# Kernel tuning notes

Measured on AMD Instinct MI355X. Metric: run time of the kernel, lower is better.

Reference implementation:

```python
import jax, jax.numpy as jnp
import numpy as np

N = 50000
NEG_SLOPE = 0.2  # PyG GATConv default negative_slope


def _gat_layer(x, src, dst, edge_attr, W, We, a_src, a_dst, a_edge, bias):
    """Single-head PyG GATConv (heads=1, concat=True, add_self_loops=True,
    fill_value='mean' for self-loop edge_attr, dropout inactive / eval mode)."""
    n = x.shape[0]
    # add self loops; self-loop edge_attr = per-feature mean of edge_attr
    loop = jnp.arange(n)
    src2 = jnp.concatenate([src, loop])
    dst2 = jnp.concatenate([dst, loop])
    ea_loop = jnp.broadcast_to(edge_attr.mean(axis=0, keepdims=True), (n, edge_attr.shape[1]))
    ea = jnp.concatenate([edge_attr, ea_loop], axis=0)          # [E', edge_dim]

    h = x @ W                                                    # [N, C_out]
    a_s = h @ a_src                                              # [N]
    a_d = h @ a_dst                                              # [N]
    a_e = (ea @ We) @ a_edge                                     # [E']

    alpha = jax.nn.leaky_relu(a_s[src2] + a_d[dst2] + a_e, NEG_SLOPE)  # [E']
    # segment softmax over incoming edges of each dst node
    amax = jax.ops.segment_max(alpha, dst2, num_segments=n)     # [N]
    ex = jnp.exp(alpha - amax[dst2])                             # [E']
    denom = jax.ops.segment_sum(ex, dst2, num_segments=n)       # [N]
    w = ex / denom[dst2]                                         # [E']

    msg = h[src2] * w[:, None]                                   # [E', C_out]
    out = jax.ops.segment_sum(msg, dst2, num_segments=n) + bias  # [N, C_out]
    return out


def setup_inputs() -> dict:
    key = jax.random.key(0)
    ks = jax.random.split(key, 16)
    E, C_in, C_h, C_out, Ed = 800000, 128, 256, 128, 8
    s = 0.05
    inp = {
        "x": jax.random.normal(ks[0], (N, C_in), dtype=jnp.float32),
        "edge_index": jax.random.randint(ks[1], (2, E), 0, N, dtype=jnp.int32),
        "edge_attr": jax.random.normal(ks[2], (E, Ed), dtype=jnp.float32),
        # layer 1 params
        "W1": jax.random.normal(ks[3], (C_in, C_h), dtype=jnp.float32) * s,
        "We1": jax.random.normal(ks[4], (Ed, C_h), dtype=jnp.float32) * s,
        "as1": jax.random.normal(ks[5], (C_h,), dtype=jnp.float32) * s,
        "ad1": jax.random.normal(ks[6], (C_h,), dtype=jnp.float32) * s,
        "ae1": jax.random.normal(ks[7], (C_h,), dtype=jnp.float32) * s,
        "b1": jnp.zeros((C_h,), dtype=jnp.float32),
        # layer 2 params
        "W2": jax.random.normal(ks[8], (C_h, C_out), dtype=jnp.float32) * s,
        "We2": jax.random.normal(ks[9], (Ed, C_out), dtype=jnp.float32) * s,
        "as2": jax.random.normal(ks[10], (C_out,), dtype=jnp.float32) * s,
        "ad2": jax.random.normal(ks[11], (C_out,), dtype=jnp.float32) * s,
        "ae2": jax.random.normal(ks[12], (C_out,), dtype=jnp.float32) * s,
        "b2": jnp.zeros((C_out,), dtype=jnp.float32),
    }
    return inp


def reference(x, edge_index, edge_attr, W1, We1, as1, ad1, ae1, b1,
              W2, We2, as2, ad2, ae2, b2):
    src, dst = edge_index[0], edge_index[1]
    h = _gat_layer(x, src, dst, edge_attr, W1, We1, as1, ad1, ae1, b1)
    h = jax.nn.relu(h)  # relu between layers, not after last
    out = _gat_layer(h, src, dst, edge_attr, W2, We2, as2, ad2, ae2, b2)
    return out
```

## Files before the change

kernel.cpp:

```cpp
#include <hip/hip_runtime.h>
#include <hip/hip_bf16.h>


#define NEG_SLOPE 0.2f

typedef unsigned short u16;
typedef short short8 __attribute__((ext_vector_type(8)));
typedef float v4f __attribute__((ext_vector_type(4)));
typedef u16 u16x8 __attribute__((ext_vector_type(8)));

__device__ __forceinline__ u16 f2bf(float f) {
    unsigned u = __float_as_uint(f);
    return (u16)((u + 0x7fffu + ((u >> 16) & 1u)) >> 16);
}
__device__ __forceinline__ float bf2f(u16 h) {
    return __uint_as_float(((unsigned)h) << 16);
}
__device__ __forceinline__ float bf_lo(int v) { return __uint_as_float(((unsigned)v) << 16); }
__device__ __forceinline__ float bf_hi(int v) { return __uint_as_float(((unsigned)v) & 0xffff0000u); }
__device__ __forceinline__ float lrelu(float x) {
    return x >= 0.f ? x : NEG_SLOPE * x;
}
__device__ __forceinline__ int ld_acq(int* p) {
    return __hip_atomic_load(p, __ATOMIC_ACQUIRE, __HIP_MEMORY_SCOPE_AGENT);
}
__device__ __forceinline__ void st_rel(int* p, int v) {
    __hip_atomic_store(p, v, __ATOMIC_RELEASE, __HIP_MEMORY_SCOPE_AGENT);
}

__global__ __launch_bounds__(256) void prep_kernel(
        const float* __restrict__ W1, u16* __restrict__ w1thi, u16* __restrict__ w1tlo,
        const float* __restrict__ W2, u16* __restrict__ w2thi, u16* __restrict__ w2tlo,
        const float* __restrict__ We1, const float* __restrict__ ae1v,
        const float* __restrict__ We2, const float* __restrict__ ae2v,
        float* __restrict__ we_vec1g, float* __restrict__ we_vec2g) {
    int tid = threadIdx.x;
    if (blockIdx.x < 256) {
        int t = blockIdx.x * 256 + tid;
        if (t < 128 * 256) {
            int k = t >> 8, m = t & 255;
            float v = W1[t];
            u16 h = f2bf(v);
            w1thi[(size_t)m * 128 + k] = h;
            w1tlo[(size_t)m * 128 + k] = f2bf(v - bf2f(h));
        } else {
            t -= 128 * 256;
            int k = t >> 7, m = t & 127;
            float v = W2[t];
            u16 h = f2bf(v);
            w2thi[(size_t)m * 256 + k] = h;
            w2tlo[(size_t)m * 256 + k] = f2bf(v - bf2f(h));
        }
        return;
    }
    __shared__ float wv[16];
    if (tid < 16) wv[tid] = 0.f;
    __syncthreads();
    {
        float a1 = ae1v[tid];
        int lane = tid & 63;
#pragma unroll
        for (int j = 0; j < 8; ++j) {
            float v = We1[j * 256 + tid] * a1;
#pragma unroll
            for (int o = 32; o; o >>= 1) v += __shfl_down(v, o);
            if (lane == 0) atomicAdd(&wv[j], v);
        }
        if (tid < 128) {
            float a2 = ae2v[tid];
#pragma unroll
            for (int j = 0; j < 8; ++j) {
                float v = We2[j * 128 + tid] * a2;
#pragma unroll
                for (int o = 32; o; o >>= 1) v += __shfl_down(v, o);
                if (lane == 0) atomicAdd(&wv[8 + j], v);
            }
        }
    }
    __syncthreads();
    if (tid < 8)  we_vec1g[tid] = wv[tid];
    else if (tid < 16) we_vec2g[tid - 8] = wv[tid];
}

#define BK 32
#define LDA 40
__global__ __launch_bounds__(256) void fat1_kernel(
        const float* __restrict__ ea, const int* __restrict__ dst,
        float* __restrict__ mean_acc, int* __restrict__ deg,
        int* __restrict__ rank, float2* __restrict__ aEe, int E,
        const float* __restrict__ we_vec1g, const float* __restrict__ we_vec2g,
        int Fb, int Gg,
        const float* __restrict__ A32,
        const u16* __restrict__ Bh_g, const u16* __restrict__ Bl_g,
        u16* __restrict__ Cb, int Nrows, int K, int M,
        const float* __restrict__ av, const float* __restrict__ bv,
        float* __restrict__ as_out, float* __restrict__ ad_out, int gx) {
    __shared__ u16 Ah[64 * LDA];
    __shared__ u16 Bh[128 * LDA];
    __shared__ u16 Bl[128 * LDA];
    __shared__ float red[8];
    int tid = threadIdx.x;
    int bid = (int)blockIdx.x;
    int mn = Fb < Gg ? Fb : Gg;
    int hid = -1, gid = -1;
    if (bid < 2 * mn) {
        if ((bid & 1) == 0) hid = bid >> 1; else gid = bid >> 1;
    } else {
        int rem = bid - 2 * mn;
        if (Fb > Gg) hid = mn + rem; else gid = mn + rem;
    }
    if (hid >= 0) {
        float wv[16];
#pragma unroll
        for (int j = 0; j < 8; ++j) { wv[j] = we_vec1g[j]; wv[8 + j] = we_vec2g[j]; }
        if (tid < 8) red[tid] = 0.f;
        __syncthreads();
        float s[8] = {0.f};
        int stride = Fb * 256;
        for (int e = hid * 256 + tid; e < E; e += stride) {
            int d = dst[e];
            const float4 v0 = *(const float4*)&ea[(size_t)e * 8];
            const float4 v1 = *(const float4*)&ea[(size_t)e * 8 + 4];
            s[0] += v0.x; s[1] += v0.y; s[2] += v0.z; s[3] += v0.w;
            s[4] += v1.x; s[5] += v1.y; s[6] += v1.z; s[7] += v1.w;
            float s1 = v0.x * wv[0] + v0.y * wv[1] + v0.z * wv[2] + v0.w * wv[3]
                     + v1.x * wv[4] + v1.y * wv[5] + v1.z * wv[6] + v1.w * wv[7];
            float s2 = v0.x * wv[8] + v0.y * wv[9] + v0.z * wv[10] + v0.w * wv[11]
                     + v1.x * wv[12] + v1.y * wv[13] + v1.z * wv[14] + v1.w * wv[15];
            aEe[e] = make_float2(s1, s2);
            rank[e] = atomicAdd(&deg[d], 1);
        }
        int lane = tid & 63;
#pragma unroll
        for (int j = 0; j < 8; ++j) {
#pragma unroll
            for (int o = 32; o; o >>= 1) s[j] += __shfl_down(s[j], o);
            if (lane == 0) atomicAdd(&red[j], s[j]);
        }
        __syncthreads();
        if (tid < 8) atomicAdd(&mean_acc[tid], red[tid]);
        return;
    }
    int lane = tid & 63;
    int wvx = tid >> 6;
    int l15 = lane & 15, quad = lane >> 4;
    int rb = (gid / gx) * 64;
    int cb = (gid % gx) * 128;

    v4f acc[8];
#pragma unroll
    for (int ni = 0; ni < 8; ++ni) acc[ni] = (v4f){0.f, 0.f, 0.f, 0.f};

    int sr  = tid >> 2;
    int sc  = (tid & 3) * 8;
    int sr2 = tid >> 1;
    int sc2 = (tid & 1) * 16;

    for (int kc = 0; kc < K; kc += BK) {
        int gr = rb + sr;
        u16x8 a0 = {0,0,0,0,0,0,0,0};
        if (gr < Nrows) {
            const float* pa = A32 + (size_t)gr * K + kc + sc;
            float4 f0 = *(const float4*)pa;
            float4 f1 = *(const float4*)(pa + 4);
            a0 = (u16x8){f2bf(f0.x), f2bf(f0.y), f2bf(f0.z), f2bf(f0.w),
                         f2bf(f1.x), f2bf(f1.y), f2bf(f1.z), f2bf(f1.w)};
        }
        size_t bb = (size_t)(cb + sr2) * K + kc + sc2;
        u16x8 b0 = *(const u16x8*)(Bh_g + bb);
        u16x8 b1 = *(const u16x8*)(Bh_g + bb + 8);
        u16x8 b2 = *(const u16x8*)(Bl_g + bb);
        u16x8 b3 = *(const u16x8*)(Bl_g + bb + 8);
        *(u16x8*)&Ah[sr * LDA + sc] = a0;
        *(u16x8*)&Bh[sr2 * LDA + sc2] = b0;
        *(u16x8*)&Bh[sr2 * LDA + sc2 + 8] = b1;
        *(u16x8*)&Bl[sr2 * LDA + sc2] = b2;
        *(u16x8*)&Bl[sr2 * LDA + sc2 + 8] = b3;
        __syncthreads();
        short8 ah = *(const short8*)&Ah[(wvx * 16 + l15) * LDA + quad * 8];
#pragma unroll
        for (int ni = 0; ni < 8; ++ni) {
            int r = (ni * 16 + l15) * LDA + quad * 8;
            short8 bhf = *(const short8*)&Bh[r];
            short8 blf = *(const short8*)&Bl[r];
            acc[ni] = __builtin_amdgcn_mfma_f32_16x16x32_bf16(ah, bhf, acc[ni], 0, 0, 0);
            acc[ni] = __builtin_amdgcn_mfma_f32_16x16x32_bf16(ah, blf, acc[ni], 0, 0, 0);
        }
        __syncthreads();
    }
#pragma unroll
    for (int ni = 0; ni < 8; ++ni)
#pragma unroll
        for (int reg = 0; reg < 4; ++reg) {
            int row = rb + wvx * 16 + quad * 4 + reg;
            if (row < Nrows)
                Cb[(size_t)row * M + cb + ni * 16 + l15] = f2bf(acc[ni][reg]);
        }
    float sd[4] = {}, dd[4] = {};
#pragma unroll
    for (int ni = 0; ni < 8; ++ni) {
        int col = cb + ni * 16 + l15;
        float a = av[col], b = bv[col];
#pragma unroll
        for (int reg = 0; reg < 4; ++reg) {
            sd[reg] += acc[ni][reg] * a;
            dd[reg] += acc[ni][reg] * b;
        }
    }
#pragma unroll
    for (int off = 1; off < 16; off <<= 1)
#pragma unroll
        for (int reg = 0; reg < 4; ++reg) {
            sd[reg] += __shfl_xor(sd[reg], off);
            dd[reg] += __shfl_xor(dd[reg], off);
        }
    if (l15 == 0) {
        int row0 = rb + wvx * 16 + quad * 4;
#pragma unroll
        for (int reg = 0; reg < 4; ++reg)
            if (row0 + reg < Nrows) {
                atomicAdd(as_out + row0 + reg, sd[reg]);
                atomicAdd(ad_out + row0 + reg, dd[reg]);
            }
    }
}

__global__ __launch_bounds__(256) void scan_fused_kernel(
        const int* __restrict__ deg, int* __restrict__ row_start,
        int* __restrict__ partials, int* __restrict__ pprefix,
        int* __restrict__ gcount, int* __restrict__ gflag, int N, int n,
        const float* __restrict__ mean_acc, float Einv,
        const float* __restrict__ we_vec1, const float* __restrict__ we_vec2,
        float* __restrict__ ae_loop) {
    __shared__ int s[256];
    __shared__ int amLast, bprefix;
    int t = threadIdx.x, bid = blockIdx.x;
    int i = bid * 256 + t;
    int v = (i < N) ? deg[i] : 0;
    s[t] = v; __syncthreads();
    for (int off = 1; off < 256; off <<= 1) {
        int u = (t >= off) ? s[t - off] : 0;
        __syncthreads();
        s[t] += u;
        __syncthreads();
    }
    int incl = s[t];
    int total = s[255];
    if (t == 0) {
        partials[bid] = total;
        __threadfence();
        int c = __hip_atomic_fetch_add(gcount, 1, __ATOMIC_ACQ_REL, __HIP_MEMORY_SCOPE_AGENT);
        amLast = (c == (int)gridDim.x - 1);
    }
    __syncthreads();
    if (amLast) {
        int G = gridDim.x;
        int pv = (t < G) ? ld_acq(&partials[t]) : 0;
        __syncthreads();
        s[t] = pv; __syncthreads();
        for (int off = 1; off < 256; off <<= 1) {
            int u = (t >= off) ? s[t - off] : 0;
            __syncthreads();
            s[t] += u;
            __syncthreads();
        }
        if (t < G) pprefix[t] = s[t] - pv;
        if (t == 0) {
            float s1 = 0.f, s2 = 0.f;
#pragma unroll
            for (int j = 0; j < 8; ++j) {
                float m = mean_acc[j] * Einv;
                s1 += m * we_vec1[j];
                s2 += m * we_vec2[j];
            }
            ae_loop[0] = s1; ae_loop[1] = s2;
        }
        __threadfence();
        __syncthreads();
        if (t == 0) st_rel(gflag, 1);
    }
    if (t == 0) {
        while (ld_acq(gflag) == 0) __builtin_amdgcn_s_sleep(2);
        bprefix = ld_acq(&pprefix[bid]);
    }
    __syncthreads();
    int ex = bprefix + incl - v;
    if (i < n) row_start[i] = ex;
}

__global__ __launch_bounds__(256) void fill_kernel(
        const int* __restrict__ src, const int* __restrict__ dst,
        const float2* __restrict__ aEe, const int* __restrict__ row_start,
        const int* __restrict__ rank,
        const float* __restrict__ asv1, const float* __restrict__ adv1,
        float4* __restrict__ epack, int E) {
    int e = blockIdx.x * 256 + threadIdx.x;
    if (e >= E) return;
    int d = dst[e];
    int s = src[e];
    int idx = row_start[d] + rank[e];
    float2 a = aEe[e];
    float w = __expf(lrelu(asv1[s] + adv1[d] + a.x));
    epack[idx] = make_float4(__int_as_float(s), w, a.y, 0.f);
}

#define LDA2 40
__global__ __launch_bounds__(256) void gemm_mfma_kernel(
        const u16* __restrict__ A_g,
        const u16* __restrict__ Bh_g, const u16* __restrict__ Bl_g,
        u16* __restrict__ Cb, int Nrows, int K, int M,
        const float* __restrict__ av, const float* __restrict__ bv,
        float* __restrict__ as_out, float* __restrict__ ad_out) {
    __shared__ u16 Ah[128 * LDA2], Bh[128 * LDA2], Bl[128 * LDA2];
    int tid = threadIdx.x;
    int lane = tid & 63;
    int wv = tid >> 6;
    int wm = wv >> 1, wn = wv & 1;
    int l15 = lane & 15, quad = lane >> 4;
    int rb = blockIdx.y * 128;
    int cb = blockIdx.x * 128;

    v4f acc[4][4];
#pragma unroll
    for (int mi = 0; mi < 4; ++mi)
#pragma unroll
        for (int ni = 0; ni < 4; ++ni) acc[mi][ni] = (v4f){0.f, 0.f, 0.f, 0.f};

    int sr = tid >> 1;
    int sc = (tid & 1) * 16;

    for (int kc = 0; kc < K; kc += BK) {
        int gr = rb + sr;
        u16x8 a0 = {0,0,0,0,0,0,0,0}, a1 = {0,0,0,0,0,0,0,0};
        if (gr < Nrows) {
            size_t ba = (size_t)gr * K + kc + sc;
            a0 = *(const u16x8*)(A_g + ba);
            a1 = *(const u16x8*)(A_g + ba + 8);
        }
        size_t bb = (size_t)(cb + sr) * K + kc + sc;
        u16x8 b0 = *(const u16x8*)(Bh_g + bb);
        u16x8 b1 = *(const u16x8*)(Bh_g + bb + 8);
        u16x8 b2 = *(const u16x8*)(Bl_g + bb);
        u16x8 b3 = *(const u16x8*)(Bl_g + bb + 8);
        *(u16x8*)&Ah[sr * LDA2 + sc] = a0;
        *(u16x8*)&Ah[sr * LDA2 + sc + 8] = a1;
        *(u16x8*)&Bh[sr * LDA2 + sc] = b0;
        *(u16x8*)&Bh[sr * LDA2 + sc + 8] = b1;
        *(u16x8*)&Bl[sr * LDA2 + sc] = b2;
        *(u16x8*)&Bl[sr * LDA2 + sc + 8] = b3;
        __syncthreads();
        short8 ah[4], bh[4], bl[4];
#pragma unroll
        for (int mi = 0; mi < 4; ++mi)
            ah[mi] = *(const short8*)&Ah[(wm * 64 + mi * 16 + l15) * LDA2 + quad * 8];
#pragma unroll
        for (int ni = 0; ni < 4; ++ni) {
            int r = (wn * 64 + ni * 16 + l15) * LDA2 + quad * 8;
            bh[ni] = *(const short8*)&Bh[r];
            bl[ni] = *(const short8*)&Bl[r];
        }
#pragma unroll
        for (int mi = 0; mi < 4; ++mi)
#pragma unroll
            for (int ni = 0; ni < 4; ++ni) {
                acc[mi][ni] = __builtin_amdgcn_mfma_f32_16x16x32_bf16(ah[mi], bh[ni], acc[mi][ni], 0, 0, 0);
                acc[mi][ni] = __builtin_amdgcn_mfma_f32_16x16x32_bf16(ah[mi], bl[ni], acc[mi][ni], 0, 0, 0);
            }
        __syncthreads();
    }
#pragma unroll
    for (int mi = 0; mi < 4; ++mi)
#pragma unroll
        for (int ni = 0; ni < 4; ++ni)
#pragma unroll
            for (int reg = 0; reg < 4; ++reg) {
                int row = rb + wm * 64 + mi * 16 + quad * 4 + reg;
                if (row < Nrows)
                    Cb[(size_t)row * M + cb + wn * 64 + ni * 16 + l15] = f2bf(acc[mi][ni][reg]);
            }
    float sd[4][4] = {}, dd[4][4] = {};
#pragma unroll
    for (int ni = 0; ni < 4; ++ni) {
        int col = cb + wn * 64 + ni * 16 + l15;
        float a = av[col], b = bv[col];
#pragma unroll
        for (int mi = 0; mi < 4; ++mi)
#pragma unroll
            for (int reg = 0; reg < 4; ++reg) {
                sd[mi][reg] += acc[mi][ni][reg] * a;
                dd[mi][reg] += acc[mi][ni][reg] * b;
            }
    }
#pragma unroll
    for (int off = 1; off < 16; off <<= 1)
#pragma unroll
        for (int mi = 0; mi < 4; ++mi)
#pragma unroll
            for (int reg = 0; reg < 4; ++reg) {
                sd[mi][reg] += __shfl_xor(sd[mi][reg], off);
                dd[mi][reg] += __shfl_xor(dd[mi][reg], off);
            }
    if (l15 == 0)
#pragma unroll
        for (int mi = 0; mi < 4; ++mi) {
            int row0 = rb + wm * 64 + mi * 16 + quad * 4;
#pragma unroll
            for (int reg = 0; reg < 4; ++reg)
                if (row0 + reg < Nrows) {
                    atomicAdd(as_out + row0 + reg, sd[mi][reg]);
                    atomicAdd(ad_out + row0 + reg, dd[mi][reg]);
                }
        }
}

__global__ __launch_bounds__(256) void agg1_kernel(const int* __restrict__ row_start,
                                                   const float4* __restrict__ epack,
                                                   const float* __restrict__ asv,
                                                   const float* __restrict__ adv,
                                                   const float* __restrict__ ae_loop,
                                                   const u16* __restrict__ Hb,
                                                   u16* __restrict__ ohi,
                                                   const float* __restrict__ bias, int N) {
    __shared__ float2 xch[4][64];
    int lane = threadIdx.x & 63;
    int wvi = threadIdx.x >> 6;
    int node = blockIdx.x * 4 + wvi;
    if (node >= N) return;
    int st = row_start[node], en = row_start[node + 1];
    float wloop = __expf(lrelu(asv[node] + adv[node] + ae_loop[0]));
    float sum = wloop;
    int half = lane >> 5;
    int hl   = lane & 31;
    float acc[8];
    {
        int4 hv = *(const int4*)(Hb + (size_t)node * 256 + hl * 8);
        float w0 = half ? 0.f : wloop;
        acc[0] = w0 * bf_lo(hv.x); acc[1] = w0 * bf_hi(hv.x);
        acc[2] = w0 * bf_lo(hv.y); acc[3] = w0 * bf_hi(hv.y);
        acc[4] = w0 * bf_lo(hv.z); acc[5] = w0 * bf_hi(hv.z);
        acc[6] = w0 * bf_lo(hv.w); acc[7] = w0 * bf_hi(hv.w);
    }
    for (int base = st; base < en; base += 64) {
        int i = base + lane;
        float w = 0.f; int sreg = 0;
        if (i < en) {
            float4 ep = epack[i];
            sreg = __float_as_int(ep.x);
            w = ep.y;
        }
        float wsum = w;
#pragma unroll
        for (int o = 1; o < 64; o <<= 1) wsum += __shfl_xor(wsum, o);
        sum += wsum;
        xch[wvi][lane] = make_float2(w, __int_as_float(sreg));
        int cnt = min(64, en - base);
        int j = 0;
        for (; j + 8 <= cnt; j += 8) {
            float2 e[4]; int4 h[4];
#pragma unroll
            for (int q = 0; q < 4; ++q) e[q] = xch[wvi][j + 2 * q + half];
#pragma unroll
            for (int q = 0; q < 4; ++q)
                h[q] = *(const int4*)(Hb + (size_t)__float_as_int(e[q].y) * 256 + hl * 8);
#pragma unroll
            for (int q = 0; q < 4; ++q) {
                float w0 = e[q].x;
                acc[0] += w0 * bf_lo(h[q].x); acc[1] += w0 * bf_hi(h[q].x);
                acc[2] += w0 * bf_lo(h[q].y); acc[3] += w0 * bf_hi(h[q].y);
                acc[4] += w0 * bf_lo(h[q].z); acc[5] += w0 * bf_hi(h[q].z);
                acc[6] += w0 * bf_lo(h[q].w); acc[7] += w0 * bf_hi(h[q].w);
            }
        }
        for (; j + 2 <= cnt; j += 2) {
            float2 e0 = xch[wvi][j + half];
            int4 h0 = *(const int4*)(Hb + (size_t)__float_as_int(e0.y) * 256 + hl * 8);
            float w0 = e0.x;
            acc[0] += w0 * bf_lo(h0.x); acc[1] += w0 * bf_hi(h0.x);
            acc[2] += w0 * bf_lo(h0.y); acc[3] += w0 * bf_hi(h0.y);
            acc[4] += w0 * bf_lo(h0.z); acc[5] += w0 * bf_hi(h0.z);
            acc[6] += w0 * bf_lo(h0.w); acc[7] += w0 * bf_hi(h0.w);
        }
        if (j < cnt && half == 0) {
            float2 e0 = xch[wvi][j];
            int4 h0 = *(const int4*)(Hb + (size_t)__float_as_int(e0.y) * 256 + hl * 8);
            float w0 = e0.x;
            acc[0] += w0 * bf_lo(h0.x); acc[1] += w0 * bf_hi(h0.x);
            acc[2] += w0 * bf_lo(h0.y); acc[3] += w0 * bf_hi(h0.y);
            acc[4] += w0 * bf_lo(h0.z); acc[5] += w0 * bf_hi(h0.z);
            acc[6] += w0 * bf_lo(h0.w); acc[7] += w0 * bf_hi(h0.w);
        }
    }
#pragma unroll
    for (int c = 0; c < 8; ++c) acc[c] += __shfl_xor(acc[c], 32);
    if (half == 0) {
        float inv = 1.f / sum;
        const float4 b0 = *(const float4*)(bias + hl * 8);
        const float4 b1 = *(const float4*)(bias + hl * 8 + 4);
        float t0 = acc[0] * inv + b0.x, t1 = acc[1] * inv + b0.y;
        float t2 = acc[2] * inv + b0.z, t3 = acc[3] * inv + b0.w;
        float t4 = acc[4] * inv + b1.x, t5 = acc[5] * inv + b1.y;
        float t6 = acc[6] * inv + b1.z, t7 = acc[7] * inv + b1.w;
        t0 = t0 > 0.f ? t0 : 0.f; t1 = t1 > 0.f ? t1 : 0.f;
        t2 = t2 > 0.f ? t2 : 0.f; t3 = t3 > 0.f ? t3 : 0.f;
        t4 = t4 > 0.f ? t4 : 0.f; t5 = t5 > 0.f ? t5 : 0.f;
        t6 = t6 > 0.f ? t6 : 0.f; t7 = t7 > 0.f ? t7 : 0.f;
        u16x8 h;
        h[0] = f2bf(t0); h[1] = f2bf(t1); h[2] = f2bf(t2); h[3] = f2bf(t3);
        h[4] = f2bf(t4); h[5] = f2bf(t5); h[6] = f2bf(t6); h[7] = f2bf(t7);
        *(u16x8*)(ohi + (size_t)node * 256 + hl * 8) = h;
    }
}

__global__ __launch_bounds__(256) void agg2_kernel(const int* __restrict__ row_start,
                                                   const float4* __restrict__ epack,
                                                   const float* __restrict__ asv,
                                                   const float* __restrict__ adv,
                                                   const float* __restrict__ ae_loop,
                                                   const u16* __restrict__ Hb,
                                                   float* __restrict__ out,
                                                   const float* __restrict__ bias, int N) {
    __shared__ float2 xch[4][64];
    int lane = threadIdx.x & 63;
    int wvi = threadIdx.x >> 6;
    int node = blockIdx.x * 4 + wvi;
    if (node >= N) return;
    int st = row_start[node], en = row_start[node + 1];
    float ad = adv[node];
    float wloop = __expf(lrelu(asv[node] + ad + ae_loop[1]));
    float sum = wloop;
    int quarter = lane >> 4;
    int hl      = lane & 15;
    float acc[8];
    {
        int4 hv = *(const int4*)(Hb + (size_t)node * 128 + hl * 8);
        float w0 = quarter ? 0.f : wloop;
        acc[0] = w0 * bf_lo(hv.x); acc[1] = w0 * bf_hi(hv.x);
        acc[2] = w0 * bf_lo(hv.y); acc[3] = w0 * bf_hi(hv.y);
        acc[4] = w0 * bf_lo(hv.z); acc[5] = w0 * bf_hi(hv.z);
        acc[6] = w0 * bf_lo(hv.w); acc[7] = w0 * bf_hi(hv.w);
    }
    for (int base = st; base < en; base += 64) {
        int i = base + lane;
        float w = 0.f; int sreg = 0;
        if (i < en) {
            float4 ep = epack[i];
            sreg = __float_as_int(ep.x);
            w = __expf(lrelu(asv[sreg] + ad + ep.z));
        }
        float wsum = w;
#pragma unroll
        for (int o = 1; o < 64; o <<= 1) wsum += __shfl_xor(wsum, o);
        sum += wsum;
        xch[wvi][lane] = make_float2(w, __int_as_float(sreg));
        int cnt = min(64, en - base);
        int j = 0;
        for (; j + 8 <= cnt; j += 8) {
            float2 e[2]; int4 h[2];
#pragma unroll
            for (int q = 0; q < 2; ++q) e[q] = xch[wvi][j + 4 * q + quarter];
#pragma unroll
            for (int q = 0; q < 2; ++q)
                h[q] = *(const int4*)(Hb + (size_t)__float_as_int(e[q].y) * 128 + hl * 8);
#pragma unroll
            for (int q = 0; q < 2; ++q) {
                float w0 = e[q].x;
                acc[0] += w0 * bf_lo(h[q].x); acc[1] += w0 * bf_hi(h[q].x);
                acc[2] += w0 * bf_lo(h[q].y); acc[3] += w0 * bf_hi(h[q].y);
                acc[4] += w0 * bf_lo(h[q].z); acc[5] += w0 * bf_hi(h[q].z);
                acc[6] += w0 * bf_lo(h[q].w); acc[7] += w0 * bf_hi(h[q].w);
            }
        }
        for (; j + 4 <= cnt; j += 4) {
            float2 e0 = xch[wvi][j + quarter];
            int4 h0 = *(const int4*)(Hb + (size_t)__float_as_int(e0.y) * 128 + hl * 8);
            float w0 = e0.x;
            acc[0] += w0 * bf_lo(h0.x); acc[1] += w0 * bf_hi(h0.x);
            acc[2] += w0 * bf_lo(h0.y); acc[3] += w0 * bf_hi(h0.y);
            acc[4] += w0 * bf_lo(h0.z); acc[5] += w0 * bf_hi(h0.z);
            acc[6] += w0 * bf_lo(h0.w); acc[7] += w0 * bf_hi(h0.w);
        }
        if (j < cnt) {
            int rem = cnt - j;
            float2 e0 = xch[wvi][j + (quarter < rem ? quarter : 0)];
            float w0 = (quarter < rem) ? e0.x : 0.f;
            int4 h0 = *(const int4*)(Hb + (size_t)__float_as_int(e0.y) * 128 + hl * 8);
            acc[0] += w0 * bf_lo(h0.x); acc[1] += w0 * bf_hi(h0.x);
            acc[2] += w0 * bf_lo(h0.y); acc[3] += w0 * bf_hi(h0.y);
            acc[4] += w0 * bf_lo(h0.z); acc[5] += w0 * bf_hi(h0.z);
            acc[6] += w0 * bf_lo(h0.w); acc[7] += w0 * bf_hi(h0.w);
        }
    }
#pragma unroll
    for (int c = 0; c < 8; ++c) {
        acc[c] += __shfl_xor(acc[c], 16);
        acc[c] += __shfl_xor(acc[c], 32);
    }
    if (quarter == 0) {
        float inv = 1.f / sum;
        const float4 b0 = *(const float4*)(bias + hl * 8);
        const float4 b1 = *(const float4*)(bias + hl * 8 + 4);
        float4 o0, o1;
        o0.x = acc[0] * inv + b0.x; o0.y = acc[1] * inv + b0.y;
        o0.z = acc[2] * inv + b0.z; o0.w = acc[3] * inv + b0.w;
        o1.x = acc[4] * inv + b1.x; o1.y = acc[5] * inv + b1.y;
        o1.z = acc[6] * inv + b1.z; o1.w = acc[7] * inv + b1.w;
        float* op = out + (size_t)node * 128 + hl * 8;
        *(float4*)op = o0;
        *(float4*)(op + 4) = o1;
    }
}

extern "C" void kernel_launch(void* const* d_in, const int* in_sizes, int n_in,
                              void* d_out, int out_size, void* d_ws, size_t ws_size,
                              hipStream_t stream) {
    const int Cin = 128, Ch = 256, Co = 128;
    const int N = in_sizes[0] / Cin;
    const int E = in_sizes[1] / 2;

    const float* x   = (const float*)d_in[0];
    const int*   src = (const int*)d_in[1];
    const int*   dst = src + E;
    const float* ea  = (const float*)d_in[2];
    const float* W1  = (const float*)d_in[3];
    const float* We1 = (const float*)d_in[4];
    const float* as1 = (const float*)d_in[5];
    const float* ad1 = (const float*)d_in[6];
    const float* ae1 = (const float*)d_in[7];
    const float* b1  = (const float*)d_in[8];
    const float* W2  = (const float*)d_in[9];
    const float* We2 = (const float*)d_in[10];
    const float* as2 = (const float*)d_in[11];
    const float* ad2 = (const float*)d_in[12];
    const float* ae2 = (const float*)d_in[13];
    const float* b2  = (const float*)d_in[14];
    float* out = (float*)d_out;

    float* ws = (float*)d_ws;
    size_t off = 0;
    u16* h1b = (u16*)(ws + off); off += (size_t)N * Ch / 2;
    u16* g1b = (u16*)(ws + off); off += (size_t)N * Ch / 2;
    float4* epack = (float4*)(ws + off); off += (size_t)E * 4;
    float2* aEe   = (float2*)(ws + off); off += (size_t)E * 2;
    int* rank     = (int*)(ws + off); off += (size_t)E;
    int* row_start = (int*)(ws + off); off += (size_t)N + 1;
    int* partials  = (int*)(ws + off); off += 256;
    int* pprefix   = (int*)(ws + off); off += 256;
    u16* w1thi = (u16*)(ws + off); off += (size_t)Cin * Ch / 2;
    u16* w1tlo = (u16*)(ws + off); off += (size_t)Cin * Ch / 2;
    u16* w2thi = (u16*)(ws + off); off += (size_t)Ch * Co / 2;
    u16* w2tlo = (u16*)(ws + off); off += (size_t)Ch * Co / 2;
    int*   deg  = (int*)(ws + off); off += (size_t)N + 1;
    float* asv1 = ws + off; off += (size_t)N;
    float* adv1 = ws + off; off += (size_t)N;
    float* asv2 = ws + off; off += (size_t)N;
    float* adv2 = ws + off; off += (size_t)N;
    float* misc = ws + off; off += 32;
    float* mean_acc = misc;
    float* we_vec1  = misc + 8;
    float* we_vec2  = misc + 16;
    float* ae_loop  = misc + 24;
    int* gcount = (int*)(ws + off); off += 1;
    int* gflag  = (int*)(ws + off); off += 1;

    const int n1 = N + 1;
    const int nscan = (n1 + 255) / 256;

    hipMemsetAsync(deg, 0, ((size_t)5 * N + 35) * sizeof(float), stream);

    prep_kernel<<<257, 256, 0, stream>>>(
        W1, w1thi, w1tlo, W2, w2thi, w2tlo,
        We1, ae1, We2, ae2, we_vec1, we_vec2);

    {
        int Fb = 1024;
        int gx = Ch / 128;
        int Gg = gx * ((N + 63) / 64);
        fat1_kernel<<<Fb + Gg, 256, 0, stream>>>(
            ea, dst, mean_acc, deg, rank, aEe, E, we_vec1, we_vec2, Fb, Gg,
            x, w1thi, w1tlo, h1b, N, Cin, Ch, as1, ad1, asv1, adv1, gx);
    }

    scan_fused_kernel<<<nscan, 256, 0, stream>>>(
        deg, row_start, partials, pprefix, gcount, gflag, N, n1,
        mean_acc, 1.0f / (float)E, we_vec1, we_vec2, ae_loop);

    fill_kernel<<<(E + 255) / 256, 256, 0, stream>>>(src, dst, aEe, row_start,
                                                     rank, asv1, adv1, epack, E);

    agg1_kernel<<<(N + 3) / 4, 256, 0, stream>>>(row_start, epack, asv1, adv1, ae_loop,
                                                 h1b, g1b, b1, N);

    u16* h2b = h1b;
    {
        dim3 grid(Co / 128, (N + 127) / 128);
        gemm_mfma_kernel<<<grid, 256, 0, stream>>>(g1b, w2thi, w2tlo, h2b, N, Ch, Co,
                                                   as2, ad2, asv2, adv2);
    }
    agg2_kernel<<<(N + 3) / 4, 256, 0, stream>>>(row_start, epack, asv2, adv2, ae_loop,
                                                 h2b, out, b2, N);
}
```

Measured before the change: 346.5 us.

## Overlap layer-2 GEMM with tail of layer-1 aggregation in fused launch

Layer-1 aggregation is split at a fixed node boundary. The first part runs alone, and a combined kernel then interleaves the remaining aggregation blocks with GEMM tiles for the rows that are already aggregated. A final small GEMM launch covers the remaining rows. The GEMM is rewritten as a direct-from-global MFMA tile of 64 rows with no LDS staging, and h2 gets its own buffer instead of reusing h1. The aim is to hide GEMM time behind the memory-bound gather and cut serialization between kernels, at the cost of a hardcoded split point and an extra buffer.

```diff
diff --git a/kernel.cpp b/kernel.cpp
--- a/kernel.cpp
+++ b/kernel.cpp
@@ -304,128 +304,13 @@
     epack[idx] = make_float4(__int_as_float(s), w, a.y, 0.f);
 }
 
-#define LDA2 40
-__global__ __launch_bounds__(256) void gemm_mfma_kernel(
-        const u16* __restrict__ A_g,
-        const u16* __restrict__ Bh_g, const u16* __restrict__ Bl_g,
-        u16* __restrict__ Cb, int Nrows, int K, int M,
-        const float* __restrict__ av, const float* __restrict__ bv,
-        float* __restrict__ as_out, float* __restrict__ ad_out) {
-    __shared__ u16 Ah[128 * LDA2], Bh[128 * LDA2], Bl[128 * LDA2];
-    int tid = threadIdx.x;
-    int lane = tid & 63;
-    int wv = tid >> 6;
-    int wm = wv >> 1, wn = wv & 1;
-    int l15 = lane & 15, quad = lane >> 4;
-    int rb = blockIdx.y * 128;
-    int cb = blockIdx.x * 128;
-
-    v4f acc[4][4];
-#pragma unroll
-    for (int mi = 0; mi < 4; ++mi)
-#pragma unroll
-        for (int ni = 0; ni < 4; ++ni) acc[mi][ni] = (v4f){0.f, 0.f, 0.f, 0.f};
-
-    int sr = tid >> 1;
-    int sc = (tid & 1) * 16;
-
-    for (int kc = 0; kc < K; kc += BK) {
-        int gr = rb + sr;
-        u16x8 a0 = {0,0,0,0,0,0,0,0}, a1 = {0,0,0,0,0,0,0,0};
-        if (gr < Nrows) {
-            size_t ba = (size_t)gr * K + kc + sc;
-            a0 = *(const u16x8*)(A_g + ba);
-            a1 = *(const u16x8*)(A_g + ba + 8);
-        }
-        size_t bb = (size_t)(cb + sr) * K + kc + sc;
-        u16x8 b0 = *(const u16x8*)(Bh_g + bb);
-        u16x8 b1 = *(const u16x8*)(Bh_g + bb + 8);
-        u16x8 b2 = *(const u16x8*)(Bl_g + bb);
-        u16x8 b3 = *(const u16x8*)(Bl_g + bb + 8);
-        *(u16x8*)&Ah[sr * LDA2 + sc] = a0;
-        *(u16x8*)&Ah[sr * LDA2 + sc + 8] = a1;
-        *(u16x8*)&Bh[sr * LDA2 + sc] = b0;
-        *(u16x8*)&Bh[sr * LDA2 + sc + 8] = b1;
-        *(u16x8*)&Bl[sr * LDA2 + sc] = b2;
-        *(u16x8*)&Bl[sr * LDA2 + sc + 8] = b3;
-        __syncthreads();
-        short8 ah[4], bh[4], bl[4];
-#pragma unroll
-        for (int mi = 0; mi < 4; ++mi)
-            ah[mi] = *(const short8*)&Ah[(wm * 64 + mi * 16 + l15) * LDA2 + quad * 8];
-#pragma unroll
-        for (int ni = 0; ni < 4; ++ni) {
-            int r = (wn * 64 + ni * 16 + l15) * LDA2 + quad * 8;
-            bh[ni] = *(const short8*)&Bh[r];
-            bl[ni] = *(const short8*)&Bl[r];
-        }
-#pragma unroll
-        for (int mi = 0; mi < 4; ++mi)
-#pragma unroll
-            for (int ni = 0; ni < 4; ++ni) {
-                acc[mi][ni] = __builtin_amdgcn_mfma_f32_16x16x32_bf16(ah[mi], bh[ni], acc[mi][ni], 0, 0, 0);
-                acc[mi][ni] = __builtin_amdgcn_mfma_f32_16x16x32_bf16(ah[mi], bl[ni], acc[mi][ni], 0, 0, 0);
-            }
-        __syncthreads();
-    }
-#pragma unroll
-    for (int mi = 0; mi < 4; ++mi)
-#pragma unroll
-        for (int ni = 0; ni < 4; ++ni)
-#pragma unroll
-            for (int reg = 0; reg < 4; ++reg) {
-                int row = rb + wm * 64 + mi * 16 + quad * 4 + reg;
-                if (row < Nrows)
-                    Cb[(size_t)row * M + cb + wn * 64 + ni * 16 + l15] = f2bf(acc[mi][ni][reg]);
-            }
-    float sd[4][4] = {}, dd[4][4] = {};
-#pragma unroll
-    for (int ni = 0; ni < 4; ++ni) {
-        int col = cb + wn * 64 + ni * 16 + l15;
-        float a = av[col], b = bv[col];
-#pragma unroll
-        for (int mi = 0; mi < 4; ++mi)
-#pragma unroll
-            for (int reg = 0; reg < 4; ++reg) {
-                sd[mi][reg] += acc[mi][ni][reg] * a;
-                dd[mi][reg] += acc[mi][ni][reg] * b;
-            }
-    }
-#pragma unroll
-    for (int off = 1; off < 16; off <<= 1)
-#pragma unroll
-        for (int mi = 0; mi < 4; ++mi)
-#pragma unroll
-            for (int reg = 0; reg < 4; ++reg) {
-                sd[mi][reg] += __shfl_xor(sd[mi][reg], off);
-                dd[mi][reg] += __shfl_xor(dd[mi][reg], off);
-            }
-    if (l15 == 0)
-#pragma unroll
-        for (int mi = 0; mi < 4; ++mi) {
-            int row0 = rb + wm * 64 + mi * 16 + quad * 4;
-#pragma unroll
-            for (int reg = 0; reg < 4; ++reg)
-                if (row0 + reg < Nrows) {
-                    atomicAdd(as_out + row0 + reg, sd[mi][reg]);
-                    atomicAdd(ad_out + row0 + reg, dd[mi][reg]);
-                }
-        }
-}
-
-__global__ __launch_bounds__(256) void agg1_kernel(const int* __restrict__ row_start,
-                                                   const float4* __restrict__ epack,
-                                                   const float* __restrict__ asv,
-                                                   const float* __restrict__ adv,
-                                                   const float* __restrict__ ae_loop,
-                                                   const u16* __restrict__ Hb,
-                                                   u16* __restrict__ ohi,
-                                                   const float* __restrict__ bias, int N) {
-    __shared__ float2 xch[4][64];
-    int lane = threadIdx.x & 63;
-    int wvi = threadIdx.x >> 6;
-    int node = blockIdx.x * 4 + wvi;
-    if (node >= N) return;
+__device__ __forceinline__ void agg1_node(
+        int node, int lane, float2* xw,
+        const int* __restrict__ row_start, const float4* __restrict__ epack,
+        const float* __restrict__ asv, const float* __restrict__ adv,
+        const float* __restrict__ ae_loop,
+        const u16* __restrict__ Hb, u16* __restrict__ ohi,
+        const float* __restrict__ bias) {
     int st = row_start[node], en = row_start[node + 1];
     float wloop = __expf(lrelu(asv[node] + adv[node] + ae_loop[0]));
     float sum = wloop;
@@ -452,13 +337,13 @@
 #pragma unroll
         for (int o = 1; o < 64; o <<= 1) wsum += __shfl_xor(wsum, o);
         sum += wsum;
-        xch[wvi][lane] = make_float2(w, __int_as_float(sreg));
-        int cnt = min(64, en - base);
+        xw[lane] = make_float2(w, __int_as_float(sreg));
+        int cnt = en - base; if (cnt > 64) cnt = 64;
         int j = 0;
         for (; j + 8 <= cnt; j += 8) {
             float2 e[4]; int4 h[4];
 #pragma unroll
-            for (int q = 0; q < 4; ++q) e[q] = xch[wvi][j + 2 * q + half];
+            for (int q = 0; q < 4; ++q) e[q] = xw[j + 2 * q + half];
 #pragma unroll
             for (int q = 0; q < 4; ++q)
                 h[q] = *(const int4*)(Hb + (size_t)__float_as_int(e[q].y) * 256 + hl * 8);
@@ -472,7 +357,7 @@
             }
         }
         for (; j + 2 <= cnt; j += 2) {
-            float2 e0 = xch[wvi][j + half];
+            float2 e0 = xw[j + half];
             int4 h0 = *(const int4*)(Hb + (size_t)__float_as_int(e0.y) * 256 + hl * 8);
             float w0 = e0.x;
             acc[0] += w0 * bf_lo(h0.x); acc[1] += w0 * bf_hi(h0.x);
@@ -481,7 +366,7 @@
             acc[6] += w0 * bf_lo(h0.w); acc[7] += w0 * bf_hi(h0.w);
         }
         if (j < cnt && half == 0) {
-            float2 e0 = xch[wvi][j];
+            float2 e0 = xw[j];
             int4 h0 = *(const int4*)(Hb + (size_t)__float_as_int(e0.y) * 256 + hl * 8);
             float w0 = e0.x;
             acc[0] += w0 * bf_lo(h0.x); acc[1] += w0 * bf_hi(h0.x);
@@ -509,6 +394,132 @@
         h[4] = f2bf(t4); h[5] = f2bf(t5); h[6] = f2bf(t6); h[7] = f2bf(t7);
         *(u16x8*)(ohi + (size_t)node * 256 + hl * 8) = h;
     }
+}
+
+__global__ __launch_bounds__(256) void agg1_kernel(
+        int n0, int ncap,
+        const int* __restrict__ row_start, const float4* __restrict__ epack,
+        const float* __restrict__ asv, const float* __restrict__ adv,
+        const float* __restrict__ ae_loop,
+        const u16* __restrict__ Hb, u16* __restrict__ ohi,
+        const float* __restrict__ bias) {
+    __shared__ float2 xch[4][64];
+    int lane = threadIdx.x & 63;
+    int wvi = threadIdx.x >> 6;
+    int node = n0 + blockIdx.x * 4 + wvi;
+    if (node >= ncap) return;
+    agg1_node(node, lane, xch[wvi], row_start, epack, asv, adv, ae_loop,
+              Hb, ohi, bias);
+}
+
+__device__ __forceinline__ void gemm2_direct_tile(
+        int rb, int Nrows, int tid,
+        const u16* __restrict__ A_g, const u16* __restrict__ Bh_g,
+        const u16* __restrict__ Bl_g, u16* __restrict__ Cb,
+        const float* __restrict__ av, const float* __restrict__ bv,
+        float* __restrict__ as_out, float* __restrict__ ad_out) {
+    const int K = 256, M = 128;
+    int lane = tid & 63;
+    int wvx = tid >> 6;
+    int l15 = lane & 15, quad = lane >> 4;
+    int arow = rb + wvx * 16 + l15;
+    const u16* pa = A_g + (size_t)arow * K + quad * 8;
+    v4f acc[8];
+#pragma unroll
+    for (int ni = 0; ni < 8; ++ni) acc[ni] = (v4f){0.f, 0.f, 0.f, 0.f};
+#pragma unroll
+    for (int kc = 0; kc < K; kc += 32) {
+        short8 ah = {0,0,0,0,0,0,0,0};
+        if (arow < Nrows) ah = *(const short8*)(pa + kc);
+#pragma unroll
+        for (int ni = 0; ni < 8; ++ni) {
+            size_t bo = (size_t)(ni * 16 + l15) * K + kc + quad * 8;
+            short8 bh = *(const short8*)(Bh_g + bo);
+            short8 bl = *(const short8*)(Bl_g + bo);
+            acc[ni] = __builtin_amdgcn_mfma_f32_16x16x32_bf16(ah, bh, acc[ni], 0, 0, 0);
+            acc[ni] = __builtin_amdgcn_mfma_f32_16x16x32_bf16(ah, bl, acc[ni], 0, 0, 0);
+        }
+    }
+#pragma unroll
+    for (int ni = 0; ni < 8; ++ni)
+#pragma unroll
+        for (int reg = 0; reg < 4; ++reg) {
+            int row = rb + wvx * 16 + quad * 4 + reg;
+            if (row < Nrows)
+                Cb[(size_t)row * M + ni * 16 + l15] = f2bf(acc[ni][reg]);
+        }
+    float sd[4] = {}, dd[4] = {};
+#pragma unroll
+    for (int ni = 0; ni < 8; ++ni) {
+        int col = ni * 16 + l15;
+        float a = av[col], b = bv[col];
+#pragma unroll
+        for (int reg = 0; reg < 4; ++reg) {
+            sd[reg] += acc[ni][reg] * a;
+            dd[reg] += acc[ni][reg] * b;
+        }
+    }
+#pragma unroll
+    for (int off = 1; off < 16; off <<= 1)
+#pragma unroll
+        for (int reg = 0; reg < 4; ++reg) {
+            sd[reg] += __shfl_xor(sd[reg], off);
+            dd[reg] += __shfl_xor(dd[reg], off);
+        }
+    if (l15 == 0) {
+        int row0 = rb + wvx * 16 + quad * 4;
+#pragma unroll
+        for (int reg = 0; reg < 4; ++reg)
+            if (row0 + reg < Nrows) {
+                atomicAdd(as_out + row0 + reg, sd[reg]);
+                atomicAdd(ad_out + row0 + reg, dd[reg]);
+            }
+    }
+}
+
+__global__ __launch_bounds__(256) void fat_ag_kernel(
+        int Ga, int n0a, int Ncap, int Gg, int r0g, int NrowsG,
+        const int* __restrict__ row_start, const float4* __restrict__ epack,
+        const float* __restrict__ asv1v, const float* __restrict__ adv1v,
+        const float* __restrict__ ae_loop,
+        const u16* __restrict__ h1b, u16* __restrict__ g1b,
+        const float* __restrict__ b1,
+        const u16* __restrict__ Ag, const u16* __restrict__ Bh_g,
+        const u16* __restrict__ Bl_g, u16* __restrict__ Cb,
+        const float* __restrict__ av, const float* __restrict__ bv,
+        float* __restrict__ asv2, float* __restrict__ adv2) {
+    __shared__ float2 xch[4][64];
+    int tid = threadIdx.x;
+    int bid = (int)blockIdx.x;
+    int mn = Ga < Gg ? Ga : Gg;
+    int aid = -1, gid = -1;
+    if (bid < 2 * mn) {
+        if ((bid & 1) == 0) aid = bid >> 1; else gid = bid >> 1;
+    } else {
+        int rem = bid - 2 * mn;
+        if (Ga > Gg) aid = mn + rem; else gid = mn + rem;
+    }
+    if (aid >= 0) {
+        int lane = tid & 63;
+        int wvi = tid >> 6;
+        int node = n0a + aid * 4 + wvi;
+        if (node >= Ncap) return;
+        agg1_node(node, lane, xch[wvi], row_start, epack, asv1v, adv1v, ae_loop,
+                  h1b, g1b, b1);
+        return;
+    }
+    gemm2_direct_tile(r0g + gid * 64, NrowsG, tid, Ag, Bh_g, Bl_g, Cb,
+                      av, bv, asv2, adv2);
+}
+
+__global__ __launch_bounds__(256) void gemm2_direct_kernel(
+        int r0, int Nrows,
+        const u16* __restrict__ Ag, const u16* __restrict__ Bh_g,
+        const u16* __restrict__ Bl_g, u16* __restrict__ Cb,
+        const float* __restrict__ av, const float* __restrict__ bv,
+        float* __restrict__ asv2, float* __restrict__ adv2) {
+    gemm2_direct_tile(r0 + (int)blockIdx.x * 64, Nrows, (int)threadIdx.x,
+                      Ag, Bh_g, Bl_g, Cb, av, bv, asv2, adv2);
 }
 
 __global__ __launch_bounds__(256) void agg2_kernel(const int* __restrict__ row_start,
@@ -639,6 +650,7 @@
     size_t off = 0;
     u16* h1b = (u16*)(ws + off); off += (size_t)N * Ch / 2;
     u16* g1b = (u16*)(ws + off); off += (size_t)N * Ch / 2;
+    u16* h2b = (u16*)(ws + off); off += (size_t)N * Co / 2;
     float4* epack = (float4*)(ws + off); off += (size_t)E * 4;
     float2* aEe   = (float2*)(ws + off); off += (size_t)E * 2;
     int* rank     = (int*)(ws + off); off += (size_t)E;
@@ -687,15 +699,24 @@
     fill_kernel<<<(E + 255) / 256, 256, 0, stream>>>(src, dst, aEe, row_start,
                                                      rank, asv1, adv1, epack, E);
 
-    agg1_kernel<<<(N + 3) / 4, 256, 0, stream>>>(row_start, epack, asv1, adv1, ae_loop,
-                                                 h1b, g1b, b1, N);
-
-    u16* h2b = h1b;
+    const int Nh = 33280;
+    agg1_kernel<<<Nh / 4, 256, 0, stream>>>(
+        0, Nh, row_start, epack, asv1, adv1, ae_loop, h1b, g1b, b1);
+
     {
-        dim3 grid(Co / 128, (N + 127) / 128);
-        gemm_mfma_kernel<<<grid, 256, 0, stream>>>(g1b, w2thi, w2tlo, h2b, N, Ch, Co,
-                                                   as2, ad2, asv2, adv2);
-    }
+        int Ga = (N - Nh + 3) / 4;
+        int Gg0 = Nh / 64;
+        fat_ag_kernel<<<Ga + Gg0, 256, 0, stream>>>(
+            Ga, Nh, N, Gg0, 0, Nh,
+            row_start, epack, asv1, adv1, ae_loop, h1b, g1b, b1,
+            g1b, w2thi, w2tlo, h2b, as2, ad2, asv2, adv2);
+    }
+    {
+        int Gg1 = (N - Nh + 63) / 64;
+        gemm2_direct_kernel<<<Gg1, 256, 0, stream>>>(
+            Nh, N, g1b, w2thi, w2tlo, h2b, as2, ad2, asv2, adv2);
+    }
+
     agg2_kernel<<<(N + 3) / 4, 256, 0, stream>>>(row_start, epack, asv2, adv2, ae_loop,
                                                  h2b, out, b2, N);
 }
```

New measurement: 422.6 us. +22.0%, slower.
